# Optimization experiments

Measured on AMD Instinct MI355X. Metric: run time of the kernel, lower is better.

## Reference

```python
import jax, jax.numpy as jnp
import numpy as np

EPS = 1e-6

def _rms(x, g):
    # RMSNorm over last dim (head_dim)
    return x * jax.lax.rsqrt(jnp.mean(x * x, axis=-1, keepdims=True) + EPS) * g

def _split_heads(x, h):
    b, l, hd = x.shape
    return x.reshape(b, l, h, hd // h).transpose(0, 2, 1, 3)  # b h l d

def setup_inputs() -> dict:
    key = jax.random.key(0)
    ks = jax.random.split(key, 10)
    B, Limg, Lip, D, Dip, Temb = 1, 2048, 512, 3072, 1280, 1280
    return {
        "ip_hidden_states": jax.random.normal(ks[0], (B, Lip, Dip), jnp.float32),
        "img_query": jax.random.normal(ks[1], (B, Limg, D), jnp.float32),
        "img_key": jax.random.normal(ks[2], (B, Limg, D), jnp.float32),
        "img_value": jax.random.normal(ks[3], (B, Limg, D), jnp.float32),
        "t_emb": jax.random.normal(ks[4], (B, Temb), jnp.float32),
        "w_ada": jax.random.normal(ks[5], (2 * Dip, Temb), jnp.float32) * 0.02,
        "b_ada": jnp.zeros((2 * Dip,), jnp.float32),
        "w_k_ip": jax.random.normal(ks[6], (D, Dip), jnp.float32) * 0.02,
        "w_v_ip": jax.random.normal(ks[7], (D, Dip), jnp.float32) * 0.02,
        "g_q": jnp.ones((128,), jnp.float32),
        "g_k": jnp.ones((128,), jnp.float32),
        "g_ipk": jnp.ones((128,), jnp.float32),
        "n_heads": 24,
    }

def reference(ip_hidden_states, img_query, img_key, img_value, t_emb,
              w_ada, b_ada, w_k_ip, w_v_ip, g_q, g_k, g_ipk, n_heads):
    # AdaLayerNorm ('normal' mode): silu + linear -> shift/scale, LayerNorm (no affine)
    e = jax.nn.silu(t_emb) @ w_ada.T + b_ada              # [B, 2*Dip]
    shift, scale = jnp.split(e, 2, axis=1)
    mu = jnp.mean(ip_hidden_states, axis=-1, keepdims=True)
    var = jnp.var(ip_hidden_states, axis=-1, keepdims=True)
    xn = (ip_hidden_states - mu) * jax.lax.rsqrt(var + EPS)
    ip_norm = xn * (1.0 + scale[:, None]) + shift[:, None]  # [B, Lip, Dip]

    ip_key = ip_norm @ w_k_ip.T                            # [B, Lip, D]
    ip_value = ip_norm @ w_v_ip.T

    q = _split_heads(img_query, n_heads)                   # [B, H, Limg, d]
    k = _split_heads(img_key, n_heads)
    v = _split_heads(img_value, n_heads)
    ipk = _split_heads(ip_key, n_heads)                    # [B, H, Lip, d]
    ipv = _split_heads(ip_value, n_heads)

    q = _rms(q, g_q)
    k = _rms(k, g_k)
    ipk = _rms(ipk, g_ipk)

    key_all = jnp.concatenate([k, ipk], axis=2)            # [B, H, Limg+Lip, d]
    val_all = jnp.concatenate([v, ipv], axis=2)

    d = q.shape[-1]
    scores = jnp.einsum('bhqd,bhkd->bhqk', q, key_all) * (1.0 / np.sqrt(d))
    probs = jax.nn.softmax(scores, axis=-1)
    out = jnp.einsum('bhqk,bhkd->bhqd', probs, val_all)    # [B, H, Limg, d]

    b, h, l, dd = out.shape
    return out.transpose(0, 2, 1, 3).reshape(b, l, h * dd)
```

## Files before the change

### kernel.cpp

```cpp
#include <hip/hip_runtime.h>
#include <math.h>

#define H    24
#define Dh   128
#define LIMG 2048
#define LIP  512
#define DM   3072
#define DIP  1280
#define LK   2560
#define EPSF 1e-6f
#define SM_SCALE 0.08838834764831845f
#define C2EXP 0.12751930f
#define THRU 90.50967f

#define EXP2F(x) __builtin_exp2f(x)

typedef __attribute__((ext_vector_type(8))) short bf16x8;
typedef __attribute__((ext_vector_type(4))) float f32x4;

typedef const unsigned int __attribute__((address_space(1))) gu32;
typedef unsigned int __attribute__((address_space(3))) lu32;

static __device__ __forceinline__ unsigned short f2bf(float x) {
  union { float f; unsigned u; } v; v.f = x;
  unsigned r = v.u + 0x7fffu + ((v.u >> 16) & 1u);
  return (unsigned short)(r >> 16);
}

static __device__ __forceinline__ float bf2f(unsigned short b) {
  union { unsigned u; float f; } v; v.u = ((unsigned)b) << 16;
  return v.f;
}

static __device__ __forceinline__ unsigned cvt_pk_bf16(float a, float b) {
  unsigned r;
  asm("v_cvt_pk_bf16_f32 %0, %1, %2" : "=v"(r) : "v"(a), "v"(b));
  return r;
}

__global__ __launch_bounds__(256) void ada_kernel(
    const float* __restrict__ t_emb, const float* __restrict__ w_ada,
    const float* __restrict__ b_ada, float* __restrict__ e) {
  int j = blockIdx.x;
  int tid = threadIdx.x;
  const float* wrow = w_ada + (long)j * DIP;
  float acc = 0.f;
  for (int k = tid; k < DIP; k += 256) {
    float t = t_emb[k];
    acc += (t / (1.f + expf(-t))) * wrow[k];
  }
#pragma unroll
  for (int m = 1; m < 64; m <<= 1) acc += __shfl_xor(acc, m, 64);
  __shared__ float red[4];
  if ((tid & 63) == 0) red[tid >> 6] = acc;
  __syncthreads();
  if (tid == 0) e[j] = red[0] + red[1] + red[2] + red[3] + b_ada[j];
}

__global__ __launch_bounds__(256) void adaln_kernel(
    const float* __restrict__ x, const float* __restrict__ e,
    unsigned short* __restrict__ ipnh, unsigned short* __restrict__ ipnl) {
  int r = blockIdx.x;
  int tid = threadIdx.x;
  const float* xr = x + (long)r * DIP;
  float v[5];
  float s = 0.f, ss = 0.f;
#pragma unroll
  for (int i = 0; i < 5; i++) {
    v[i] = xr[tid + i * 256];
    s += v[i];
    ss += v[i] * v[i];
  }
#pragma unroll
  for (int m = 1; m < 64; m <<= 1) {
    s += __shfl_xor(s, m, 64);
    ss += __shfl_xor(ss, m, 64);
  }
  __shared__ float rs_[4], rss_[4];
  if ((tid & 63) == 0) { rs_[tid >> 6] = s; rss_[tid >> 6] = ss; }
  __syncthreads();
  s = rs_[0] + rs_[1] + rs_[2] + rs_[3];
  ss = rss_[0] + rss_[1] + rss_[2] + rss_[3];
  float mu = s * (1.f / DIP);
  float var = ss * (1.f / DIP) - mu * mu;
  float rstd = rsqrtf(var + EPSF);
  unsigned short* oh = ipnh + (long)r * DIP;
  unsigned short* ol = ipnl + (long)r * DIP;
#pragma unroll
  for (int i = 0; i < 5; i++) {
    int c = tid + i * 256;
    float o = (v[i] - mu) * rstd * (1.f + e[DIP + c]) + e[c];
    unsigned short hb = f2bf(o);
    oh[c] = hb;
    ol[c] = f2bf(o - bf2f(hb));
  }
}

__global__ __launch_bounds__(256) void prep_kernel(
    const float* __restrict__ k_in, const float* __restrict__ v_in,
    const float* __restrict__ g_k,
    unsigned short* __restrict__ Kb, unsigned short* __restrict__ Vt) {
  __shared__ unsigned short Vls[128][33];
  int h = blockIdx.y, l0 = blockIdx.x * 32;
  int tid = threadIdx.x;
  int r = tid >> 3, c = tid & 7;
  const float* ksrc = k_in + (long)(l0 + r) * DM + h * Dh + c * 16;
  const float* vsrc = v_in + (long)(l0 + r) * DM + h * Dh + c * 16;
  float kv[16], vv[16];
  float ssq = 0.f;
#pragma unroll
  for (int i = 0; i < 4; i++) {
    float4 a = *(const float4*)(ksrc + i * 4);
    float4 b = *(const float4*)(vsrc + i * 4);
    kv[i*4+0]=a.x; kv[i*4+1]=a.y; kv[i*4+2]=a.z; kv[i*4+3]=a.w;
    vv[i*4+0]=b.x; vv[i*4+1]=b.y; vv[i*4+2]=b.z; vv[i*4+3]=b.w;
    ssq += a.x*a.x + a.y*a.y + a.z*a.z + a.w*a.w;
  }
  ssq += __shfl_xor(ssq, 1, 8);
  ssq += __shfl_xor(ssq, 2, 8);
  ssq += __shfl_xor(ssq, 4, 8);
  float rstd = rsqrtf(ssq * (1.f / Dh) + EPSF);
  unsigned short kb[16];
#pragma unroll
  for (int i = 0; i < 16; i++) kb[i] = f2bf(kv[i] * rstd * g_k[c * 16 + i]);
  unsigned short* kdst = Kb + ((long)h * LK + l0 + r) * Dh + c * 16;
  *(uint4*)(kdst) = *(uint4*)(kb);
  *(uint4*)(kdst + 8) = *(uint4*)(kb + 8);
#pragma unroll
  for (int i = 0; i < 16; i++) Vls[c * 16 + i][r] = f2bf(vv[i]);
  __syncthreads();
  if (tid < 128) {
    int d = tid;
    unsigned short ov[32];
#pragma unroll
    for (int j = 0; j < 32; j++) ov[j] = Vls[d][j];
    unsigned short* vdst = Vt + ((long)h * 80 + (l0 >> 5)) * 4096 + d * 32;
    *(uint4*)(vdst)      = *(uint4*)(ov);
    *(uint4*)(vdst + 8)  = *(uint4*)(ov + 8);
    *(uint4*)(vdst + 16) = *(uint4*)(ov + 16);
    *(uint4*)(vdst + 24) = *(uint4*)(ov + 24);
  }
}

__global__ __launch_bounds__(256) void proj_kernel(
    const unsigned short* __restrict__ Ah, const unsigned short* __restrict__ Al,
    const float* __restrict__ Wk, const float* __restrict__ Wv,
    const float* __restrict__ g_ipk,
    unsigned short* __restrict__ Kb, unsigned short* __restrict__ Vt) {
  __shared__ __align__(16) unsigned short lds_u[24576];
  const float* W = blockIdx.z ? Wv : Wk;
  int h = blockIdx.y;
  int m0 = blockIdx.x * 64;
  int tid = threadIdx.x;
  int w = tid >> 6, lane = tid & 63;
  int m = lane & 15, quad = lane >> 4;

  const float* wrow = W + (long)(h * Dh + (tid & 127)) * DIP + ((tid >> 7) << 3);
  const unsigned short* garow_h = Ah + (long)(m0 + lane) * DIP + w * 8;
  const unsigned short* garow_l = Al + (long)(m0 + lane) * DIP + w * 8;

  f32x4 acc[8];
#pragma unroll
  for (int i = 0; i < 8; i++) acc[i] = (f32x4){0.f, 0.f, 0.f, 0.f};

  float4 wa = *(const float4*)(wrow);
  float4 wb = *(const float4*)(wrow + 4);
  float4 wc = *(const float4*)(wrow + 16);
  float4 wd = *(const float4*)(wrow + 20);

  auto stagek = [&](int b, int k0) {
    float cur[16] = {wa.x, wa.y, wa.z, wa.w, wb.x, wb.y, wb.z, wb.w,
                     wc.x, wc.y, wc.z, wc.w, wd.x, wd.y, wd.z, wd.w};
    if (k0 + 32 < DIP) {
      wa = *(const float4*)(wrow + k0 + 32);
      wb = *(const float4*)(wrow + k0 + 36);
      wc = *(const float4*)(wrow + k0 + 48);
      wd = *(const float4*)(wrow + k0 + 52);
    }
    unsigned hw[8], lw[8];
#pragma unroll
    for (int i = 0; i < 8; i++) {
      float a = cur[2 * i], b = cur[2 * i + 1];
      unsigned hword = cvt_pk_bf16(a, b);
      union { unsigned u; float f; } la, lb;
      la.u = hword << 16;
      lb.u = hword & 0xffff0000u;
      unsigned lword = cvt_pk_bf16(a - la.f, b - lb.f);
      hw[i] = hword; lw[i] = lword;
    }
    unsigned short* AhsB = lds_u + b * 12288;
    unsigned short* AlsB = AhsB + 2048;
    unsigned short* WhsB = AhsB + 4096;
    unsigned short* WlsB = AhsB + 8192;
    __builtin_amdgcn_global_load_lds((gu32*)(garow_h + k0), (lu32*)(AhsB + w * 512), 16, 0, 0);
    __builtin_amdgcn_global_load_lds((gu32*)(garow_l + k0), (lu32*)(AlsB + w * 512), 16, 0, 0);
    uint4 q;
    q.x = hw[0]; q.y = hw[1]; q.z = hw[2]; q.w = hw[3];
    *(uint4*)(WhsB + tid * 8) = q;
    q.x = lw[0]; q.y = lw[1]; q.z = lw[2]; q.w = lw[3];
    *(uint4*)(WlsB + tid * 8) = q;
    q.x = hw[4]; q.y = hw[5]; q.z = hw[6]; q.w = hw[7];
    *(uint4*)(WhsB + (tid + 256) * 8) = q;
    q.x = lw[4]; q.y = lw[5]; q.z = lw[6]; q.w = lw[7];
    *(uint4*)(WlsB + (tid + 256) * 8) = q;
  };

  stagek(0, 0);
  __syncthreads();
  int buf = 0;
#pragma unroll 1
  for (int k0 = 0; k0 < DIP; k0 += 32) {
    if (k0 + 32 < DIP) stagek(buf ^ 1, k0 + 32);
    unsigned short* AhsB = lds_u + buf * 12288;
    unsigned short* AlsB = AhsB + 2048;
    unsigned short* WhsB = AhsB + 4096;
    unsigned short* WlsB = AhsB + 8192;
    bf16x8 ahf = *(const bf16x8*)(AhsB + ((quad << 6) + (w << 4) + m) * 8);
    bf16x8 alf = *(const bf16x8*)(AlsB + ((quad << 6) + (w << 4) + m) * 8);
#pragma unroll
    for (int nt = 0; nt < 8; nt++) {
      bf16x8 bhf = *(const bf16x8*)(WhsB + ((quad << 7) + (nt << 4) + m) * 8);
      bf16x8 blf = *(const bf16x8*)(WlsB + ((quad << 7) + (nt << 4) + m) * 8);
      acc[nt] = __builtin_amdgcn_mfma_f32_16x16x32_bf16(ahf, bhf, acc[nt], 0, 0, 0);
      acc[nt] = __builtin_amdgcn_mfma_f32_16x16x32_bf16(ahf, blf, acc[nt], 0, 0, 0);
      acc[nt] = __builtin_amdgcn_mfma_f32_16x16x32_bf16(alf, bhf, acc[nt], 0, 0, 0);
    }
    __syncthreads();
    buf ^= 1;
  }

  if (blockIdx.z == 0) {
    float gkv[8];
#pragma unroll
    for (int nt = 0; nt < 8; nt++) gkv[nt] = g_ipk[nt * 16 + m];
#pragma unroll
    for (int r = 0; r < 4; r++) {
      float ssq = 0.f;
#pragma unroll
      for (int nt = 0; nt < 8; nt++) ssq += acc[nt][r] * acc[nt][r];
      ssq += __shfl_xor(ssq, 1, 16);
      ssq += __shfl_xor(ssq, 2, 16);
      ssq += __shfl_xor(ssq, 4, 16);
      ssq += __shfl_xor(ssq, 8, 16);
      float rstd = rsqrtf(ssq * (1.f / Dh) + EPSF);
      long row = (long)h * LK + LIMG + m0 + w * 16 + quad * 4 + r;
#pragma unroll
      for (int nt = 0; nt < 8; nt++)
        Kb[row * Dh + nt * 16 + m] = f2bf(acc[nt][r] * rstd * gkv[nt]);
    }
  } else {
    int l0q = LIMG + m0 + w * 16 + quad * 4;
    unsigned short* vbase = Vt + ((long)h * 80 + (l0q >> 5)) * 4096 + (l0q & 31);
#pragma unroll
    for (int nt = 0; nt < 8; nt++) {
      ushort4 o;
      o.x = f2bf(acc[nt][0]); o.y = f2bf(acc[nt][1]);
      o.z = f2bf(acc[nt][2]); o.w = f2bf(acc[nt][3]);
      *(ushort4*)(vbase + (nt * 16 + m) * 32) = o;
    }
  }
}

__global__ __launch_bounds__(256, 4) void flash_kernel(
    const float* __restrict__ q_in, const float* __restrict__ g_q,
    const unsigned short* __restrict__ Kb, const unsigned short* __restrict__ Vt,
    float* __restrict__ out) {
  __shared__ __align__(16) unsigned char lds[16384 + 16384 + 5120];
  unsigned short* Ks = (unsigned short*)lds;
  unsigned short* Vs = (unsigned short*)(lds + 16384);
  unsigned short* Ps = (unsigned short*)(lds + 32768);
  int tid = threadIdx.x;
  int w = tid >> 6, lid = tid & 63;
  int m = lid & 15, quad = lid >> 4;
  int id = blockIdx.x;
  int sidx = id >> 3;
  int h = (id & 7) * 3 + (sidx >> 5);
  int q0 = (sidx & 31) * 64;
  int qrow = q0 + w * 16 + m;

  bf16x8 aq[4];
  {
    float qf[4][8];
    float ssq = 0.f;
    const float* qsrc = q_in + (long)qrow * DM + h * Dh + quad * 8;
#pragma unroll
    for (int ks = 0; ks < 4; ks++) {
      float4 a = *(const float4*)(qsrc + ks * 32);
      float4 b = *(const float4*)(qsrc + ks * 32 + 4);
      qf[ks][0]=a.x; qf[ks][1]=a.y; qf[ks][2]=a.z; qf[ks][3]=a.w;
      qf[ks][4]=b.x; qf[ks][5]=b.y; qf[ks][6]=b.z; qf[ks][7]=b.w;
      ssq += a.x*a.x + a.y*a.y + a.z*a.z + a.w*a.w;
      ssq += b.x*b.x + b.y*b.y + b.z*b.z + b.w*b.w;
    }
    ssq += __shfl_xor(ssq, 16, 64);
    ssq += __shfl_xor(ssq, 32, 64);
    float rstd = rsqrtf(ssq * (1.f / Dh) + EPSF);
    const float* gq = g_q + quad * 8;
#pragma unroll
    for (int ks = 0; ks < 4; ks++) {
      float4 ga = *(const float4*)(gq + ks * 32);
      float4 gb = *(const float4*)(gq + ks * 32 + 4);
      float gg[8] = {ga.x, ga.y, ga.z, ga.w, gb.x, gb.y, gb.z, gb.w};
#pragma unroll
      for (int j = 0; j < 8; j++)
        aq[ks][j] = (short)f2bf(qf[ks][j] * rstd * gg[j]);
    }
  }

  const unsigned short* KbH = Kb + (long)h * LK * Dh;
  const unsigned short* VtH = Vt + (long)h * 80 * 4096;
  unsigned short* Pw = Ps + w * 640;

  f32x4 acc_o[8];
#pragma unroll
  for (int i = 0; i < 8; i++) acc_o[i] = (f32x4){0.f, 0.f, 0.f, 0.f};
  float mrun = -INFINITY;
  float lrun = 0.f;

  int s0 = w * 128 + lid, s1 = s0 + 64;
  int rK0 = s0 >> 4, cK0 = (s0 & 15) ^ (rK0 & 15);
  int rK1 = s1 >> 4, cK1 = (s1 & 15) ^ (rK1 & 15);
  const unsigned short* pK0 = KbH + (long)rK0 * Dh + cK0 * 8;
  const unsigned short* pK1 = KbH + (long)rK1 * Dh + cK1 * 8;
  int dV0 = s0 >> 2, cV0 = (s0 & 3) ^ ((dV0 >> 1) & 3);
  int dV1 = s1 >> 2, cV1 = (s1 & 3) ^ ((dV1 >> 1) & 3);
  const unsigned short* pV0 = VtH + dV0 * 32 + cV0 * 8;
  const unsigned short* pV1 = VtH + dV1 * 32 + cV1 * 8;

  auto stage = [&](int b) {
    unsigned short* KsB = Ks + b * 4096;
    unsigned short* VsB = Vs + b * 4096;
    __builtin_amdgcn_global_load_lds((gu32*)pK0, (lu32*)(KsB + (w * 128) * 8), 16, 0, 0);
    __builtin_amdgcn_global_load_lds((gu32*)pK1, (lu32*)(KsB + (w * 128 + 64) * 8), 16, 0, 0);
    __builtin_amdgcn_global_load_lds((gu32*)pV0, (lu32*)(VsB + (w * 128) * 8), 16, 0, 0);
    __builtin_amdgcn_global_load_lds((gu32*)pV1, (lu32*)(VsB + (w * 128 + 64) * 8), 16, 0, 0);
    pK0 += 4096; pK1 += 4096;
    pV0 += 4096; pV1 += 4096;
  };

  auto compute = [&](const unsigned short* KsB, const unsigned short* VsB) {
    f32x4 sc[2];
    sc[0] = (f32x4){0.f, 0.f, 0.f, 0.f};
    sc[1] = (f32x4){0.f, 0.f, 0.f, 0.f};
    __builtin_amdgcn_s_setprio(1);
#pragma unroll
    for (int t = 0; t < 2; t++)
#pragma unroll
      for (int ks = 0; ks < 4; ks++) {
        int rr = t * 16 + m;
        int g = (ks * 4 + quad) ^ m;
        bf16x8 bk = *(const bf16x8*)(KsB + rr * 128 + g * 8);
        sc[t] = __builtin_amdgcn_mfma_f32_16x16x32_bf16(bk, aq[ks], sc[t], 0, 0, 0);
      }
    __builtin_amdgcn_s_setprio(0);

    float pv[8] = {sc[0][0], sc[0][1], sc[0][2], sc[0][3],
                   sc[1][0], sc[1][1], sc[1][2], sc[1][3]};
    float p[8];
#pragma unroll
    for (int j = 0; j < 8; j++) p[j] = EXP2F((pv[j] - mrun) * C2EXP);

    float t0 = fmaxf(fmaxf(pv[0], pv[1]), fmaxf(pv[2], pv[3]));
    float t1 = fmaxf(fmaxf(pv[4], pv[5]), fmaxf(pv[6], pv[7]));
    float tmax = fmaxf(t0, t1);
    tmax = fmaxf(tmax, __shfl_xor(tmax, 16, 64));
    tmax = fmaxf(tmax, __shfl_xor(tmax, 32, 64));
    if (!__all(tmax <= mrun + THRU)) {
      float mnew = fmaxf(mrun, tmax);
      float al = EXP2F((mrun - mnew) * C2EXP);
      mrun = mnew;
#pragma unroll
      for (int j = 0; j < 8; j++) p[j] = EXP2F((pv[j] - mrun) * C2EXP);
      lrun *= al;
      float alr[4];
#pragma unroll
      for (int r = 0; r < 4; r++) alr[r] = __shfl(al, quad * 4 + r, 16);
#pragma unroll
      for (int dt = 0; dt < 8; dt++) {
        acc_o[dt][0] *= alr[0]; acc_o[dt][1] *= alr[1];
        acc_o[dt][2] *= alr[2]; acc_o[dt][3] *= alr[3];
      }
    }
    lrun += (p[0] + p[1]) + (p[2] + p[3]) + (p[4] + p[5]) + (p[6] + p[7]);

    uint2 pka, pkb;
    pka.x = cvt_pk_bf16(p[0], p[1]);
    pka.y = cvt_pk_bf16(p[2], p[3]);
    pkb.x = cvt_pk_bf16(p[4], p[5]);
    pkb.y = cvt_pk_bf16(p[6], p[7]);
    *(uint2*)(Pw + m * 40 + quad * 4) = pka;
    *(uint2*)(Pw + m * 40 + 16 + quad * 4) = pkb;
    bf16x8 ap = *(const bf16x8*)(Pw + m * 40 + quad * 8);

    __builtin_amdgcn_s_setprio(1);
#pragma unroll
    for (int dt = 0; dt < 8; dt++) {
      bf16x8 bv = *(const bf16x8*)(VsB + ((dt * 16 + m) * 4 + (quad ^ ((m >> 1) & 3))) * 8);
      acc_o[dt] = __builtin_amdgcn_mfma_f32_16x16x32_bf16(ap, bv, acc_o[dt], 0, 0, 0);
    }
    __builtin_amdgcn_s_setprio(0);
  };

  stage(0);
  __syncthreads();
#pragma unroll 1
  for (int jt = 0; jt < LK / 32; jt += 2) {
    stage(1);
    compute(Ks, Vs);
    __syncthreads();
    if (jt + 2 < LK / 32) stage(0);
    compute(Ks + 4096, Vs + 4096);
    __syncthreads();
  }

  lrun += __shfl_xor(lrun, 16, 64);
  lrun += __shfl_xor(lrun, 32, 64);
  float inv = 1.f / lrun;
  float ilr[4];
#pragma unroll
  for (int r = 0; r < 4; r++) ilr[r] = __shfl(inv, quad * 4 + r, 16);
#pragma unroll
  for (int dt = 0; dt < 8; dt++)
#pragma unroll
    for (int r = 0; r < 4; r++)
      out[(long)(q0 + w * 16 + quad * 4 + r) * DM + h * Dh + dt * 16 + m] =
          acc_o[dt][r] * ilr[r];
}

extern "C" void kernel_launch(void* const* d_in, const int* in_sizes, int n_in,
                              void* d_out, int out_size, void* d_ws, size_t ws_size,
                              hipStream_t stream) {
  const float* ip_hidden = (const float*)d_in[0];
  const float* img_q     = (const float*)d_in[1];
  const float* img_k     = (const float*)d_in[2];
  const float* img_v     = (const float*)d_in[3];
  const float* t_emb     = (const float*)d_in[4];
  const float* w_ada     = (const float*)d_in[5];
  const float* b_ada     = (const float*)d_in[6];
  const float* w_k_ip    = (const float*)d_in[7];
  const float* w_v_ip    = (const float*)d_in[8];
  const float* g_q       = (const float*)d_in[9];
  const float* g_k       = (const float*)d_in[10];
  const float* g_ipk     = (const float*)d_in[11];

  char* base = (char*)d_ws;
  float* e = (float*)base;
  unsigned short* ipnh = (unsigned short*)(base + 16384);
  unsigned short* ipnl = (unsigned short*)(base + 1327104);
  unsigned short* Kb   = (unsigned short*)(base + 2637824);
  unsigned short* Vt   = Kb + (size_t)H * LK * Dh;
  float* out = (float*)d_out;

  ada_kernel<<<2 * DIP, 256, 0, stream>>>(t_emb, w_ada, b_ada, e);
  adaln_kernel<<<LIP, 256, 0, stream>>>(ip_hidden, e, ipnh, ipnl);
  prep_kernel<<<dim3(LIMG / 32, H), 256, 0, stream>>>(img_k, img_v, g_k, Kb, Vt);
  proj_kernel<<<dim3(LIP / 64, H, 2), 256, 0, stream>>>(ipnh, ipnl, w_k_ip, w_v_ip,
                                                        g_ipk, Kb, Vt);
  flash_kernel<<<dim3(768), 256, 0, stream>>>(img_q, g_q, Kb, Vt, out);
}
```

Before: 368.4 us.

## Merge ada and K/V prep kernels; halve proj tile rows for more blocks

The ada linear and the K/V RMSNorm/transpose prep become one launch with a block-index split, which removes a launch and lets the two independent jobs overlap. The projection kernel now uses 32-row tiles with a 2x2 warp layout and a padded W layout in LDS. This doubles the grid to 768 blocks for better CU occupancy. The K RMSNorm now needs a cross-warp reduction through LDS with an extra barrier, and each block stages the W tile for fewer rows.

```diff
diff --git a/kernel.cpp b/kernel.cpp
--- a/kernel.cpp
+++ b/kernel.cpp
@@ -38,23 +38,69 @@
   return r;
 }
 
-__global__ __launch_bounds__(256) void ada_kernel(
+__global__ __launch_bounds__(256) void pre_kernel(
     const float* __restrict__ t_emb, const float* __restrict__ w_ada,
-    const float* __restrict__ b_ada, float* __restrict__ e) {
-  int j = blockIdx.x;
+    const float* __restrict__ b_ada, float* __restrict__ e,
+    const float* __restrict__ k_in, const float* __restrict__ v_in,
+    const float* __restrict__ g_k,
+    unsigned short* __restrict__ Kb, unsigned short* __restrict__ Vt) {
+  __shared__ unsigned short Vls[128][33];
+  __shared__ float red[4];
   int tid = threadIdx.x;
-  const float* wrow = w_ada + (long)j * DIP;
-  float acc = 0.f;
-  for (int k = tid; k < DIP; k += 256) {
-    float t = t_emb[k];
-    acc += (t / (1.f + expf(-t))) * wrow[k];
-  }
-#pragma unroll
-  for (int m = 1; m < 64; m <<= 1) acc += __shfl_xor(acc, m, 64);
-  __shared__ float red[4];
-  if ((tid & 63) == 0) red[tid >> 6] = acc;
+  if (blockIdx.x < 2560) {
+    int j = blockIdx.x;
+    const float* wrow = w_ada + (long)j * DIP;
+    float acc = 0.f;
+    for (int k = tid; k < DIP; k += 256) {
+      float t = t_emb[k];
+      acc += (t / (1.f + expf(-t))) * wrow[k];
+    }
+#pragma unroll
+    for (int mm = 1; mm < 64; mm <<= 1) acc += __shfl_xor(acc, mm, 64);
+    if ((tid & 63) == 0) red[tid >> 6] = acc;
+    __syncthreads();
+    if (tid == 0) e[j] = red[0] + red[1] + red[2] + red[3] + b_ada[j];
+    return;
+  }
+  int pid = blockIdx.x - 2560;
+  int h = pid >> 6, l0 = (pid & 63) * 32;
+  int r = tid >> 3, c = tid & 7;
+  const float* ksrc = k_in + (long)(l0 + r) * DM + h * Dh + c * 16;
+  const float* vsrc = v_in + (long)(l0 + r) * DM + h * Dh + c * 16;
+  float kv[16], vv[16];
+  float ssq = 0.f;
+#pragma unroll
+  for (int i = 0; i < 4; i++) {
+    float4 a = *(const float4*)(ksrc + i * 4);
+    float4 b = *(const float4*)(vsrc + i * 4);
+    kv[i*4+0]=a.x; kv[i*4+1]=a.y; kv[i*4+2]=a.z; kv[i*4+3]=a.w;
+    vv[i*4+0]=b.x; vv[i*4+1]=b.y; vv[i*4+2]=b.z; vv[i*4+3]=b.w;
+    ssq += a.x*a.x + a.y*a.y + a.z*a.z + a.w*a.w;
+  }
+  ssq += __shfl_xor(ssq, 1, 8);
+  ssq += __shfl_xor(ssq, 2, 8);
+  ssq += __shfl_xor(ssq, 4, 8);
+  float rstd = rsqrtf(ssq * (1.f / Dh) + EPSF);
+  unsigned short kb[16];
+#pragma unroll
+  for (int i = 0; i < 16; i++) kb[i] = f2bf(kv[i] * rstd * g_k[c * 16 + i]);
+  unsigned short* kdst = Kb + ((long)h * LK + l0 + r) * Dh + c * 16;
+  *(uint4*)(kdst) = *(uint4*)(kb);
+  *(uint4*)(kdst + 8) = *(uint4*)(kb + 8);
+#pragma unroll
+  for (int i = 0; i < 16; i++) Vls[c * 16 + i][r] = f2bf(vv[i]);
   __syncthreads();
-  if (tid == 0) e[j] = red[0] + red[1] + red[2] + red[3] + b_ada[j];
+  if (tid < 128) {
+    int d = tid;
+    unsigned short ov[32];
+#pragma unroll
+    for (int j = 0; j < 32; j++) ov[j] = Vls[d][j];
+    unsigned short* vdst = Vt + ((long)h * 80 + (l0 >> 5)) * 4096 + d * 32;
+    *(uint4*)(vdst)      = *(uint4*)(ov);
+    *(uint4*)(vdst + 8)  = *(uint4*)(ov + 8);
+    *(uint4*)(vdst + 16) = *(uint4*)(ov + 16);
+    *(uint4*)(vdst + 24) = *(uint4*)(ov + 24);
+  }
 }
 
 __global__ __launch_bounds__(256) void adaln_kernel(
@@ -96,72 +142,30 @@
   }
 }
 
-__global__ __launch_bounds__(256) void prep_kernel(
-    const float* __restrict__ k_in, const float* __restrict__ v_in,
-    const float* __restrict__ g_k,
-    unsigned short* __restrict__ Kb, unsigned short* __restrict__ Vt) {
-  __shared__ unsigned short Vls[128][33];
-  int h = blockIdx.y, l0 = blockIdx.x * 32;
-  int tid = threadIdx.x;
-  int r = tid >> 3, c = tid & 7;
-  const float* ksrc = k_in + (long)(l0 + r) * DM + h * Dh + c * 16;
-  const float* vsrc = v_in + (long)(l0 + r) * DM + h * Dh + c * 16;
-  float kv[16], vv[16];
-  float ssq = 0.f;
-#pragma unroll
-  for (int i = 0; i < 4; i++) {
-    float4 a = *(const float4*)(ksrc + i * 4);
-    float4 b = *(const float4*)(vsrc + i * 4);
-    kv[i*4+0]=a.x; kv[i*4+1]=a.y; kv[i*4+2]=a.z; kv[i*4+3]=a.w;
-    vv[i*4+0]=b.x; vv[i*4+1]=b.y; vv[i*4+2]=b.z; vv[i*4+3]=b.w;
-    ssq += a.x*a.x + a.y*a.y + a.z*a.z + a.w*a.w;
-  }
-  ssq += __shfl_xor(ssq, 1, 8);
-  ssq += __shfl_xor(ssq, 2, 8);
-  ssq += __shfl_xor(ssq, 4, 8);
-  float rstd = rsqrtf(ssq * (1.f / Dh) + EPSF);
-  unsigned short kb[16];
-#pragma unroll
-  for (int i = 0; i < 16; i++) kb[i] = f2bf(kv[i] * rstd * g_k[c * 16 + i]);
-  unsigned short* kdst = Kb + ((long)h * LK + l0 + r) * Dh + c * 16;
-  *(uint4*)(kdst) = *(uint4*)(kb);
-  *(uint4*)(kdst + 8) = *(uint4*)(kb + 8);
-#pragma unroll
-  for (int i = 0; i < 16; i++) Vls[c * 16 + i][r] = f2bf(vv[i]);
-  __syncthreads();
-  if (tid < 128) {
-    int d = tid;
-    unsigned short ov[32];
-#pragma unroll
-    for (int j = 0; j < 32; j++) ov[j] = Vls[d][j];
-    unsigned short* vdst = Vt + ((long)h * 80 + (l0 >> 5)) * 4096 + d * 32;
-    *(uint4*)(vdst)      = *(uint4*)(ov);
-    *(uint4*)(vdst + 8)  = *(uint4*)(ov + 8);
-    *(uint4*)(vdst + 16) = *(uint4*)(ov + 16);
-    *(uint4*)(vdst + 24) = *(uint4*)(ov + 24);
-  }
-}
-
 __global__ __launch_bounds__(256) void proj_kernel(
     const unsigned short* __restrict__ Ah, const unsigned short* __restrict__ Al,
     const float* __restrict__ Wk, const float* __restrict__ Wv,
     const float* __restrict__ g_ipk,
     unsigned short* __restrict__ Kb, unsigned short* __restrict__ Vt) {
-  __shared__ __align__(16) unsigned short lds_u[24576];
+  __shared__ __align__(16) unsigned short lds_u[22528];
   const float* W = blockIdx.z ? Wv : Wk;
   int h = blockIdx.y;
-  int m0 = blockIdx.x * 64;
+  int m0 = blockIdx.x * 32;
   int tid = threadIdx.x;
   int w = tid >> 6, lane = tid & 63;
   int m = lane & 15, quad = lane >> 4;
-
-  const float* wrow = W + (long)(h * Dh + (tid & 127)) * DIP + ((tid >> 7) << 3);
-  const unsigned short* garow_h = Ah + (long)(m0 + lane) * DIP + w * 8;
-  const unsigned short* garow_l = Al + (long)(m0 + lane) * DIP + w * 8;
-
-  f32x4 acc[8];
-#pragma unroll
-  for (int i = 0; i < 8; i++) acc[i] = (f32x4){0.f, 0.f, 0.f, 0.f};
+  int rowg = w & 1, colg = w >> 1;
+
+  int wn = tid & 127, wg = tid >> 7;
+  const float* wrow = W + (long)(h * Dh + wn) * DIP + wg * 8;
+  const unsigned short* gasrc =
+      ((w < 2) ? Ah : Al) + (long)(m0 + (lane & 31)) * DIP +
+      ((w & 1) * 2 + (lane >> 5)) * 8;
+  int adst = ((w < 2) ? 0 : 1024) + (w & 1) * 512;
+
+  f32x4 acc[4];
+#pragma unroll
+  for (int i = 0; i < 4; i++) acc[i] = (f32x4){0.f, 0.f, 0.f, 0.f};
 
   float4 wa = *(const float4*)(wrow);
   float4 wb = *(const float4*)(wrow + 4);
@@ -180,29 +184,27 @@
     unsigned hw[8], lw[8];
 #pragma unroll
     for (int i = 0; i < 8; i++) {
-      float a = cur[2 * i], b = cur[2 * i + 1];
-      unsigned hword = cvt_pk_bf16(a, b);
+      float a = cur[2 * i], b2 = cur[2 * i + 1];
+      unsigned hword = cvt_pk_bf16(a, b2);
       union { unsigned u; float f; } la, lb;
       la.u = hword << 16;
       lb.u = hword & 0xffff0000u;
-      unsigned lword = cvt_pk_bf16(a - la.f, b - lb.f);
+      unsigned lword = cvt_pk_bf16(a - la.f, b2 - lb.f);
       hw[i] = hword; lw[i] = lword;
     }
-    unsigned short* AhsB = lds_u + b * 12288;
-    unsigned short* AlsB = AhsB + 2048;
-    unsigned short* WhsB = AhsB + 4096;
-    unsigned short* WlsB = AhsB + 8192;
-    __builtin_amdgcn_global_load_lds((gu32*)(garow_h + k0), (lu32*)(AhsB + w * 512), 16, 0, 0);
-    __builtin_amdgcn_global_load_lds((gu32*)(garow_l + k0), (lu32*)(AlsB + w * 512), 16, 0, 0);
+    unsigned short* B = lds_u + b * 11264;
+    __builtin_amdgcn_global_load_lds((gu32*)(gasrc + k0), (lu32*)(B + adst), 16, 0, 0);
+    unsigned short* Whs = B + 2048;
+    unsigned short* Wls = B + 6656;
     uint4 q;
     q.x = hw[0]; q.y = hw[1]; q.z = hw[2]; q.w = hw[3];
-    *(uint4*)(WhsB + tid * 8) = q;
+    *(uint4*)(Whs + wn * 36 + wg * 8) = q;
     q.x = lw[0]; q.y = lw[1]; q.z = lw[2]; q.w = lw[3];
-    *(uint4*)(WlsB + tid * 8) = q;
+    *(uint4*)(Wls + wn * 36 + wg * 8) = q;
     q.x = hw[4]; q.y = hw[5]; q.z = hw[6]; q.w = hw[7];
-    *(uint4*)(WhsB + (tid + 256) * 8) = q;
+    *(uint4*)(Whs + wn * 36 + (wg + 2) * 8) = q;
     q.x = lw[4]; q.y = lw[5]; q.z = lw[6]; q.w = lw[7];
-    *(uint4*)(WlsB + (tid + 256) * 8) = q;
+    *(uint4*)(Wls + wn * 36 + (wg + 2) * 8) = q;
   };
 
   stagek(0, 0);
@@ -211,16 +213,16 @@
 #pragma unroll 1
   for (int k0 = 0; k0 < DIP; k0 += 32) {
     if (k0 + 32 < DIP) stagek(buf ^ 1, k0 + 32);
-    unsigned short* AhsB = lds_u + buf * 12288;
-    unsigned short* AlsB = AhsB + 2048;
-    unsigned short* WhsB = AhsB + 4096;
-    unsigned short* WlsB = AhsB + 8192;
-    bf16x8 ahf = *(const bf16x8*)(AhsB + ((quad << 6) + (w << 4) + m) * 8);
-    bf16x8 alf = *(const bf16x8*)(AlsB + ((quad << 6) + (w << 4) + m) * 8);
-#pragma unroll
-    for (int nt = 0; nt < 8; nt++) {
-      bf16x8 bhf = *(const bf16x8*)(WhsB + ((quad << 7) + (nt << 4) + m) * 8);
-      bf16x8 blf = *(const bf16x8*)(WlsB + ((quad << 7) + (nt << 4) + m) * 8);
+    unsigned short* B = lds_u + buf * 11264;
+    bf16x8 ahf = *(const bf16x8*)(B + quad * 256 + (rowg * 16 + m) * 8);
+    bf16x8 alf = *(const bf16x8*)(B + 1024 + quad * 256 + (rowg * 16 + m) * 8);
+    unsigned short* Whs = B + 2048;
+    unsigned short* Wls = B + 6656;
+#pragma unroll
+    for (int nt = 0; nt < 4; nt++) {
+      int n = colg * 64 + nt * 16 + m;
+      bf16x8 bhf = *(const bf16x8*)(Whs + n * 36 + quad * 8);
+      bf16x8 blf = *(const bf16x8*)(Wls + n * 36 + quad * 8);
       acc[nt] = __builtin_amdgcn_mfma_f32_16x16x32_bf16(ahf, bhf, acc[nt], 0, 0, 0);
       acc[nt] = __builtin_amdgcn_mfma_f32_16x16x32_bf16(ahf, blf, acc[nt], 0, 0, 0);
       acc[nt] = __builtin_amdgcn_mfma_f32_16x16x32_bf16(alf, bhf, acc[nt], 0, 0, 0);
@@ -230,33 +232,47 @@
   }
 
   if (blockIdx.z == 0) {
-    float gkv[8];
-#pragma unroll
-    for (int nt = 0; nt < 8; nt++) gkv[nt] = g_ipk[nt * 16 + m];
+    float rmsp[4];
 #pragma unroll
     for (int r = 0; r < 4; r++) {
       float ssq = 0.f;
 #pragma unroll
-      for (int nt = 0; nt < 8; nt++) ssq += acc[nt][r] * acc[nt][r];
+      for (int nt = 0; nt < 4; nt++) ssq += acc[nt][r] * acc[nt][r];
       ssq += __shfl_xor(ssq, 1, 16);
       ssq += __shfl_xor(ssq, 2, 16);
       ssq += __shfl_xor(ssq, 4, 16);
       ssq += __shfl_xor(ssq, 8, 16);
+      rmsp[r] = ssq;
+    }
+    float* rb = (float*)lds_u;
+    if (m == 0) {
+#pragma unroll
+      for (int r = 0; r < 4; r++)
+        rb[colg * 32 + rowg * 16 + quad * 4 + r] = rmsp[r];
+    }
+    __syncthreads();
+#pragma unroll
+    for (int r = 0; r < 4; r++) {
+      int rowi = rowg * 16 + quad * 4 + r;
+      float ssq = rb[rowi] + rb[32 + rowi];
       float rstd = rsqrtf(ssq * (1.f / Dh) + EPSF);
-      long row = (long)h * LK + LIMG + m0 + w * 16 + quad * 4 + r;
-#pragma unroll
-      for (int nt = 0; nt < 8; nt++)
-        Kb[row * Dh + nt * 16 + m] = f2bf(acc[nt][r] * rstd * gkv[nt]);
+      long row = (long)h * LK + LIMG + m0 + rowi;
+#pragma unroll
+      for (int nt = 0; nt < 4; nt++) {
+        int col = colg * 64 + nt * 16 + m;
+        Kb[row * Dh + col] = f2bf(acc[nt][r] * rstd * g_ipk[col]);
+      }
     }
   } else {
-    int l0q = LIMG + m0 + w * 16 + quad * 4;
+    int l0q = LIMG + m0 + rowg * 16 + quad * 4;
     unsigned short* vbase = Vt + ((long)h * 80 + (l0q >> 5)) * 4096 + (l0q & 31);
 #pragma unroll
-    for (int nt = 0; nt < 8; nt++) {
+    for (int nt = 0; nt < 4; nt++) {
+      int col = colg * 64 + nt * 16 + m;
       ushort4 o;
       o.x = f2bf(acc[nt][0]); o.y = f2bf(acc[nt][1]);
       o.z = f2bf(acc[nt][2]); o.w = f2bf(acc[nt][3]);
-      *(ushort4*)(vbase + (nt * 16 + m) * 32) = o;
+      *(ushort4*)(vbase + col * 32) = o;
     }
   }
 }
@@ -451,10 +467,10 @@
   unsigned short* Vt   = Kb + (size_t)H * LK * Dh;
   float* out = (float*)d_out;
 
-  ada_kernel<<<2 * DIP, 256, 0, stream>>>(t_emb, w_ada, b_ada, e);
+  pre_kernel<<<4096, 256, 0, stream>>>(t_emb, w_ada, b_ada, e,
+                                       img_k, img_v, g_k, Kb, Vt);
   adaln_kernel<<<LIP, 256, 0, stream>>>(ip_hidden, e, ipnh, ipnl);
-  prep_kernel<<<dim3(LIMG / 32, H), 256, 0, stream>>>(img_k, img_v, g_k, Kb, Vt);
-  proj_kernel<<<dim3(LIP / 64, H, 2), 256, 0, stream>>>(ipnh, ipnl, w_k_ip, w_v_ip,
-                                                        g_ipk, Kb, Vt);
+  proj_kernel<<<dim3(16, 24, 2), 256, 0, stream>>>(ipnh, ipnl, w_k_ip, w_v_ip,
+                                                   g_ipk, Kb, Vt);
   flash_kernel<<<dim3(768), 256, 0, stream>>>(img_q, g_q, Kb, Vt, out);
 }
```

Measured after the change: 455.1 us. 1.24x slower.
